# Optimization experiments

Hardware: AMD Instinct MI355X
Metric: run time of the kernel (lower is better)

Reference implementation:

```python
import jax, jax.numpy as jnp
import numpy as np

B, A = 64, 128          # batch, number of annotations (source length)
H, E, V = 512, 512, 32000  # hidden_size, embedding_size, vocab_size


def setup_inputs() -> dict:
    key = jax.random.key(0)
    ks = jax.random.split(key, 12)
    def w(k, shape):
        return (jax.random.normal(k, shape, jnp.float32) * 0.02)
    return {
        "hidden_state": jax.random.normal(ks[0], (B, H), jnp.float32),
        "annotations": jax.random.normal(ks[1], (B, A, 2 * H), jnp.float32),
        # Wa: Linear(3H -> H), ReLU, Linear(H -> 1)
        "Wa1_w": w(ks[2], (3 * H, H)), "Wa1_b": jnp.zeros((H,), jnp.float32),
        "Wa2_w": w(ks[3], (H, 1)),     "Wa2_b": jnp.zeros((1,), jnp.float32),
        # Wf: Linear(H+E+2H -> H//2), ReLU, Linear(H//2 -> H)
        "Wf1_w": w(ks[4], (H + E + 2 * H, H // 2)), "Wf1_b": jnp.zeros((H // 2,), jnp.float32),
        "Wf2_w": w(ks[5], (H // 2, H)),             "Wf2_b": jnp.zeros((H,), jnp.float32),
        # Wg: Linear(E+H+2H -> E//2), ReLU, Linear(E//2 -> E)
        "Wg1_w": w(ks[6], (E + H + 2 * H, E // 2)), "Wg1_b": jnp.zeros((E // 2,), jnp.float32),
        "Wg2_w": w(ks[7], (E // 2, E)),             "Wg2_b": jnp.zeros((E,), jnp.float32),
        # fc: Linear(E -> V)
        "fc_w": w(ks[8], (E, V)), "fc_b": jnp.zeros((V,), jnp.float32),
        "decode_length": 64,
    }


def reference(hidden_state, annotations,
              Wa1_w, Wa1_b, Wa2_w, Wa2_b,
              Wf1_w, Wf1_b, Wf2_w, Wf2_b,
              Wg1_w, Wg1_b, Wg2_w, Wg2_b,
              fc_w, fc_b, decode_length):
    h_dim = hidden_state.shape[-1]
    # concat([s, ann]) @ Wa1 is linear: precompute annotation part once (same math).
    ann_proj = jnp.einsum('bad,dh->bah', annotations, Wa1_w[h_dim:]) + Wa1_b  # [B,A,H]
    Wa1_s = Wa1_w[:h_dim]            # [H,H] part applied to the decoder state
    y0 = jnp.zeros((hidden_state.shape[0], Wg2_w.shape[1]), hidden_state.dtype)

    def step(carry, _):
        s, y = carry
        # attention energies: MLP on concat([s, annotation])
        hid = jax.nn.relu(jnp.einsum('bh,hk->bk', s, Wa1_s)[:, None, :] + ann_proj)  # [B,A,H]
        e = jnp.einsum('bah,h->ba', hid, Wa2_w[:, 0]) + Wa2_b[0]                     # [B,A]
        attn = jax.nn.softmax(e, axis=1)
        c = jnp.einsum('ba,bad->bd', attn, annotations)                              # [B,2H]
        # f: new hidden state
        s_new = jax.nn.relu(jnp.concatenate([s, y, c], -1) @ Wf1_w + Wf1_b) @ Wf2_w + Wf2_b
        # g: prediction embedding
        y_new = jax.nn.relu(jnp.concatenate([y, s_new, c], -1) @ Wg1_w + Wg1_b) @ Wg2_w + Wg2_b
        return (s_new, y_new), y_new

    _, ys = jax.lax.scan(step, (hidden_state, y0), None, length=decode_length)
    outputs = jnp.transpose(ys, (1, 0, 2))  # [B,T,E]
    return outputs @ fc_w + fc_b            # [B,T,V]
```

## Files before the change

kernel.cpp:

```cpp
#include <hip/hip_runtime.h>

typedef unsigned short US;
typedef unsigned int   UI;
typedef __bf16 bf16x8 __attribute__((ext_vector_type(8)));
typedef float  f32x4  __attribute__((ext_vector_type(4)));

#define BB 64
#define AA 128
#define HH 512
#define TT 64
#define VV 32000

__device__ __forceinline__ US f2bf(float f) {
  UI u = __builtin_bit_cast(UI, f);
  UI r = (u + 0x7fffu + ((u >> 16) & 1u)) >> 16;
  return (US)r;
}
__device__ __forceinline__ float bflo(UI u){ return __builtin_bit_cast(float, u << 16); }
__device__ __forceinline__ float bfhi(UI u){ return __builtin_bit_cast(float, u & 0xffff0000u); }

__device__ __forceinline__ float dot8(uint4 w, const float* __restrict__ x){
  float a = 0.f;
  a += x[0]*bflo(w.x); a += x[1]*bfhi(w.x);
  a += x[2]*bflo(w.y); a += x[3]*bfhi(w.y);
  a += x[4]*bflo(w.z); a += x[5]*bfhi(w.z);
  a += x[6]*bflo(w.w); a += x[7]*bfhi(w.w);
  return a;
}

__global__ void copy_f(float* o, const float* i, int n){
  int x = blockIdx.x*blockDim.x + threadIdx.x; if (x < n) o[x] = i[x];
}
__global__ void cast4_k(US* o, const float* in, int n4){
  int x = blockIdx.x*blockDim.x + threadIdx.x;
  if (x < n4){
    float4 v = ((const float4*)in)[x];
    ushort4 r; r.x=f2bf(v.x); r.y=f2bf(v.y); r.z=f2bf(v.z); r.w=f2bf(v.w);
    ((ushort4*)o)[x] = r;
  }
}
__global__ void tcast_k(US* __restrict__ out, const float* __restrict__ in,
                        int R, int C, int in_stride){
  __shared__ float tile[32][33];
  int r0 = blockIdx.x*32, c0 = blockIdx.y*32;
  int tx = threadIdx.x, ty = threadIdx.y;
  #pragma unroll
  for (int k=0;k<4;k++)
    tile[tx][ty+8*k] = in[(long)(c0+ty+8*k)*in_stride + r0 + tx];
  __syncthreads();
  #pragma unroll
  for (int k=0;k<4;k++)
    out[(long)(r0+ty+8*k)*C + c0 + tx] = f2bf(tile[ty+8*k][tx]);
}
__global__ void w2g_k(US* __restrict__ W2gT, const float* __restrict__ Wf2,
                      const float* __restrict__ Wg1){
  int j2 = blockIdx.x, j = threadIdx.x;
  float a = 0.f;
  for (int n=0;n<HH;n++) a += Wf2[j*HH + n] * Wg1[(512+n)*256 + j2];
  W2gT[j2*256 + j] = f2bf(a);
}
__global__ void bg1p_k(float* out, const float* Wg1_b, const float* Wf2_b,
                       const float* Wg1){
  int j2 = threadIdx.x;
  float a = Wg1_b[j2];
  for (int n=0;n<HH;n++) a += Wf2_b[n]*Wg1[(512+n)*256 + j2];
  out[j2] = a;
}

template<int OUT_BF16>
__global__ __launch_bounds__(256) void gemm_bt(
    const US* __restrict__ A, const US* __restrict__ Bt, void* __restrict__ Cv,
    const float* __restrict__ bias, int M, int N, int K,
    long Az, long Bz, long Cz)
{
  const long zb = blockIdx.z;
  A  += zb*Az;  Bt += zb*Bz;
  __shared__ __align__(16) US lA[128*64];
  __shared__ __align__(16) US lB[128*64];
  const int tid = threadIdx.x, lane = tid & 63, w = tid >> 6;
  const int wr = w >> 1, wc = w & 1;
  const int tm = blockIdx.x, tn = blockIdx.y;
  f32x4 acc[4][4] = {};
  for (int kt = 0; kt < K; kt += 64) {
    __syncthreads();
    #pragma unroll
    for (int i=0;i<4;i++){
      int ci = tid + 256*i; int r = ci>>3, o = (ci&7)*8;
      *(uint4*)&lA[r*64+o] = *(const uint4*)&A [(long)(tm*128+r)*K + kt + o];
      *(uint4*)&lB[r*64+o] = *(const uint4*)&Bt[(long)(tn*128+r)*K + kt + o];
    }
    __syncthreads();
    #pragma unroll
    for (int ks=0; ks<2; ++ks){
      bf16x8 af[4], bfr[4];
      #pragma unroll
      for(int m=0;m<4;m++){
        uint4 t = *(const uint4*)&lA[(wr*64+m*16+(lane&15))*64 + ks*32 + (lane>>4)*8];
        af[m] = __builtin_bit_cast(bf16x8, t);
      }
      #pragma unroll
      for(int n=0;n<4;n++){
        uint4 t = *(const uint4*)&lB[(wc*64+n*16+(lane&15))*64 + ks*32 + (lane>>4)*8];
        bfr[n] = __builtin_bit_cast(bf16x8, t);
      }
      #pragma unroll
      for(int m=0;m<4;m++)
        #pragma unroll
        for(int n=0;n<4;n++)
          acc[m][n] = __builtin_amdgcn_mfma_f32_16x16x32_bf16(af[m], bfr[n], acc[m][n], 0,0,0);
    }
  }
  #pragma unroll
  for(int m=0;m<4;m++){
    #pragma unroll
    for(int n=0;n<4;n++){
      const int col = tn*128 + wc*64 + n*16 + (lane&15);
      const float bv = bias ? bias[col] : 0.f;
      #pragma unroll
      for(int r=0;r<4;r++){
        const int row = tm*128 + wr*64 + m*16 + (lane>>4)*4 + r;
        const float v = acc[m][n][r] + bv;
        if (OUT_BF16) ((US*)Cv)  [zb*Cz + (long)row*N + col] = f2bf(v);
        else          ((float*)Cv)[zb*Cz + (long)row*N + col] = v;
      }
    }
  }
}

__device__ __forceinline__ void bbar(int* cnt, int target){
  __syncthreads();
  if (threadIdx.x == 0){
    __threadfence();
    __hip_atomic_fetch_add(cnt, 1, __ATOMIC_RELEASE, __HIP_MEMORY_SCOPE_AGENT);
    while (__hip_atomic_load(cnt, __ATOMIC_ACQUIRE, __HIP_MEMORY_SCOPE_AGENT) < target)
      __builtin_amdgcn_s_sleep(2);
  }
  __syncthreads();
}

__global__ __launch_bounds__(512) void scan_k(
  float* __restrict__ S, float* __restrict__ Y, float* __restrict__ TMP,
  float* __restrict__ E, float* __restrict__ U, float* __restrict__ V,
  int* __restrict__ cnt,
  const US* __restrict__ Wa1sT, const US* __restrict__ Wg2T,
  const US* __restrict__ annproj, const US* __restrict__ annFt, const US* __restrict__ annGt,
  const US* __restrict__ Wf1syT, const US* __restrict__ Wf2T,
  const US* __restrict__ Wg1yT, const US* __restrict__ W2gT,
  const float* __restrict__ bg1p, const float* __restrict__ wa2g,
  const float* __restrict__ Wf1_b, const float* __restrict__ Wf2_b,
  const float* __restrict__ Wg2_b,
  US* __restrict__ ys)
{
  const int b = blockIdx.x & 63, q = blockIdx.x >> 6;
  const int tid = threadIdx.x;
  __shared__ float s_l[512], y_l[512], tmp_l[512], v_l[256], u_l[256];
  __shared__ float p_l[128], aF_l[64], aG_l[64], wa2[512], red_l[4];
  wa2[tid] = wa2g[tid];
  float* Sb = S + b*512;  float* Yb = Y + b*512;  float* Tb = TMP + b*512;
  float* Eb = E + b*128;  float* Ub = U + b*256;  float* Vb = V + b*256;
  int* cb = cnt + b*32;
  int bt = 0;

  for (int t = 0; t <= TT; ++t) {
    if (t > 0 && tid < 256) v_l[tid] = Vb[tid];
    s_l[tid] = Sb[tid];
    __syncthreads();
    {
      const int n_loc = tid >> 2, kq = tid & 3;
      const int n = q*128 + n_loc;
      if (t > 0) {
        const US* wrow = Wg2T + n*256 + kq*64;
        const float* x = &v_l[kq*64];
        float p = 0.f;
        #pragma unroll
        for (int i=0;i<8;i++) p += dot8(*(const uint4*)&wrow[i*8], &x[i*8]);
        p += __shfl_xor(p, 1); p += __shfl_xor(p, 2);
        if (kq == 0) {
          float yv = p + Wg2_b[n];
          Yb[n] = yv;
          ys[((long)b*TT + (t-1))*512 + n] = f2bf(yv);
        }
      }
      if (t == TT) break;
      {
        const US* wrow = Wa1sT + n*512 + kq*128;
        const float* x = &s_l[kq*128];
        float p = 0.f;
        #pragma unroll
        for (int i=0;i<16;i++) p += dot8(*(const uint4*)&wrow[i*8], &x[i*8]);
        p += __shfl_xor(p, 1); p += __shfl_xor(p, 2);
        if (kq == 0) Tb[n] = p;
      }
    }
    bt += 4; bbar(cb, bt);

    tmp_l[tid] = Tb[tid];
    __syncthreads();
    {
      const int a_loc = tid >> 4, hq = tid & 15;
      const int a = q*32 + a_loc;
      const US* prow = annproj + ((long)b*AA + a)*512 + hq*32;
      float p = 0.f;
      #pragma unroll
      for (int i=0;i<4;i++){
        uint4 wv = *(const uint4*)&prow[i*8];
        const int h = hq*32 + i*8;
        float tv;
        tv = tmp_l[h+0]+bflo(wv.x); p += fmaxf(tv,0.f)*wa2[h+0];
        tv = tmp_l[h+1]+bfhi(wv.x); p += fmaxf(tv,0.f)*wa2[h+1];
        tv = tmp_l[h+2]+bflo(wv.y); p += fmaxf(tv,0.f)*wa2[h+2];
        tv = tmp_l[h+3]+bfhi(wv.y); p += fmaxf(tv,0.f)*wa2[h+3];
        tv = tmp_l[h+4]+bflo(wv.z); p += fmaxf(tv,0.f)*wa2[h+4];
        tv = tmp_l[h+5]+bfhi(wv.z); p += fmaxf(tv,0.f)*wa2[h+5];
        tv = tmp_l[h+6]+bflo(wv.w); p += fmaxf(tv,0.f)*wa2[h+6];
        tv = tmp_l[h+7]+bfhi(wv.w); p += fmaxf(tv,0.f)*wa2[h+7];
      }
      p += __shfl_xor(p,1); p += __shfl_xor(p,2); p += __shfl_xor(p,4); p += __shfl_xor(p,8);
      if (hq == 0) Eb[a] = p;
    }
    bt += 4; bbar(cb, bt);

    float ev = -1e30f;
    if (tid < 128){ ev = Eb[tid]; p_l[tid] = ev; }
    y_l[tid] = Yb[tid];
    __syncthreads();
    float mloc = ev;
    #pragma unroll
    for (int o=32;o;o>>=1) mloc = fmaxf(mloc, __shfl_xor(mloc,o));
    if (tid==0)  red_l[0]=mloc;
    if (tid==64) red_l[1]=mloc;
    __syncthreads();
    const float mx = fmaxf(red_l[0], red_l[1]);
    float dloc = 0.f;
    if (tid < 128){ float pe = expf(ev - mx); p_l[tid] = pe; dloc = pe; }
    #pragma unroll
    for (int o=32;o;o>>=1) dloc += __shfl_xor(dloc,o);
    if (tid==0)  red_l[2]=dloc;
    if (tid==64) red_l[3]=dloc;
    __syncthreads();
    const float dinv = 1.f/(red_l[2]+red_l[3]);
    {
      const int j_loc = tid>>3, aq = tid&7;
      const int j = q*64 + j_loc;
      const US* fr = annFt + ((long)b*256 + j)*AA + aq*16;
      const US* gr = annGt + ((long)b*256 + j)*AA + aq*16;
      float pF=0.f, pG=0.f;
      #pragma unroll
      for (int i=0;i<2;i++){
        pF += dot8(*(const uint4*)&fr[i*8], &p_l[aq*16 + i*8]);
        pG += dot8(*(const uint4*)&gr[i*8], &p_l[aq*16 + i*8]);
      }
      pF += __shfl_xor(pF,1); pF += __shfl_xor(pF,2); pF += __shfl_xor(pF,4);
      pG += __shfl_xor(pG,1); pG += __shfl_xor(pG,2); pG += __shfl_xor(pG,4);
      if (aq==0){ aF_l[j_loc]=pF; aG_l[j_loc]=pG; }
    }
    __syncthreads();
    {
      const int j_loc = tid>>3, kq = tid&7;
      const int j = q*64 + j_loc;
      const US* wrow = Wf1syT + (long)j*1024 + kq*128;
      float p = 0.f;
      #pragma unroll
      for (int i=0;i<16;i++){
        const int k = kq*128 + i*8;
        const float* x = (k < 512) ? &s_l[k] : &y_l[k-512];
        p += dot8(*(const uint4*)&wrow[i*8], x);
      }
      p += __shfl_xor(p,1); p += __shfl_xor(p,2); p += __shfl_xor(p,4);
      if (kq==0) Ub[j] = fmaxf(p + aF_l[j_loc]*dinv + Wf1_b[j], 0.f);
    }
    bt += 4; bbar(cb, bt);

    if (tid < 256) u_l[tid] = Ub[tid];
    __syncthreads();
    {
      const int n_loc = tid>>2, kq = tid&3;
      const int n = q*128 + n_loc;
      const US* wrow = Wf2T + n*256 + kq*64;
      const float* x = &u_l[kq*64];
      float p = 0.f;
      #pragma unroll
      for (int i=0;i<8;i++) p += dot8(*(const uint4*)&wrow[i*8], &x[i*8]);
      p += __shfl_xor(p,1); p += __shfl_xor(p,2);
      if (kq==0) Sb[n] = p + Wf2_b[n];
    }
    {
      const int j2_loc = tid>>3, kq = tid&7;
      const int j2 = q*64 + j2_loc;
      const US* wy = Wg1yT + (long)j2*512 + kq*64;
      const US* wu = W2gT + j2*256 + kq*32;
      float p = 0.f;
      #pragma unroll
      for (int i=0;i<8;i++) p += dot8(*(const uint4*)&wy[i*8], &y_l[kq*64 + i*8]);
      #pragma unroll
      for (int i=0;i<4;i++) p += dot8(*(const uint4*)&wu[i*8], &u_l[kq*32 + i*8]);
      p += __shfl_xor(p,1); p += __shfl_xor(p,2); p += __shfl_xor(p,4);
      if (kq==0) Vb[j2] = fmaxf(p + aG_l[j2_loc]*dinv + bg1p[j2], 0.f);
    }
    bt += 4; bbar(cb, bt);
  }
}

extern "C" void kernel_launch(void* const* d_in, const int* in_sizes, int n_in,
                              void* d_out, int out_size, void* d_ws, size_t ws_size,
                              hipStream_t stream)
{
  (void)in_sizes; (void)n_in; (void)out_size; (void)ws_size;
  const float* hidden = (const float*)d_in[0];
  const float* ann    = (const float*)d_in[1];
  const float* Wa1_w  = (const float*)d_in[2];
  const float* Wa1_b  = (const float*)d_in[3];
  const float* Wa2_w  = (const float*)d_in[4];
  const float* Wf1_w  = (const float*)d_in[6];
  const float* Wf1_b  = (const float*)d_in[7];
  const float* Wf2_w  = (const float*)d_in[8];
  const float* Wf2_b  = (const float*)d_in[9];
  const float* Wg1_w  = (const float*)d_in[10];
  const float* Wg1_b  = (const float*)d_in[11];
  const float* Wg2_w  = (const float*)d_in[12];
  const float* Wg2_b  = (const float*)d_in[13];
  const float* fc_w   = (const float*)d_in[14];
  const float* fc_b   = (const float*)d_in[15];

  char* ws = (char*)d_ws;
  size_t off = 0;
  auto alloc = [&](size_t bytes)->char*{ char* p = ws + off; off += (bytes + 255) & ~255ULL; return p; };
  int*   cnt   = (int*)  alloc(64*32*4);
  float* Y     = (float*)alloc(64*512*4);
  float* S     = (float*)alloc(64*512*4);
  float* TMP   = (float*)alloc(64*512*4);
  float* E     = (float*)alloc(64*128*4);
  float* U     = (float*)alloc(64*256*4);
  float* V     = (float*)alloc(64*256*4);
  float* BG1P  = (float*)alloc(256*4);
  US* Wa1sT  = (US*)alloc(512*512*2);
  US* WannT  = (US*)alloc(512*1024*2);
  US* Wf1cT  = (US*)alloc(256*1024*2);
  US* Wg1cT  = (US*)alloc(256*1024*2);
  US* Wf1syT = (US*)alloc(256*1024*2);
  US* Wf2T   = (US*)alloc(512*256*2);
  US* Wg1yT  = (US*)alloc(256*512*2);
  US* Wg2T   = (US*)alloc(512*256*2);
  US* W2gT   = (US*)alloc(256*256*2);
  US* annbf  = (US*)alloc((size_t)64*128*1024*2);
  US* annproj= (US*)alloc((size_t)64*128*512*2);
  US* annFt  = (US*)alloc((size_t)64*256*128*2);
  US* annGt  = (US*)alloc((size_t)64*256*128*2);
  US* ysbf   = (US*)alloc((size_t)64*64*512*2);
  US* fcwT   = (US*)alloc((size_t)32000*512*2);

  hipMemsetAsync(d_ws, 0, 64*32*4 + 64*512*4, stream);
  copy_f<<<64, 512, 0, stream>>>(S, hidden, 64*512);
  cast4_k<<<8192, 256, 0, stream>>>(annbf, ann, 64*128*1024/4);

  dim3 tb(32,8);
  tcast_k<<<dim3(16,16),  tb, 0, stream>>>(Wa1sT,  Wa1_w,            512, 512,  512);
  tcast_k<<<dim3(16,32),  tb, 0, stream>>>(WannT,  Wa1_w + 512*512,  512, 1024, 512);
  tcast_k<<<dim3(8,32),   tb, 0, stream>>>(Wf1cT,  Wf1_w + 1024*256, 256, 1024, 256);
  tcast_k<<<dim3(8,32),   tb, 0, stream>>>(Wg1cT,  Wg1_w + 1024*256, 256, 1024, 256);
  tcast_k<<<dim3(8,32),   tb, 0, stream>>>(Wf1syT, Wf1_w,            256, 1024, 256);
  tcast_k<<<dim3(16,8),   tb, 0, stream>>>(Wf2T,   Wf2_w,            512, 256,  512);
  tcast_k<<<dim3(8,16),   tb, 0, stream>>>(Wg1yT,  Wg1_w,            256, 512,  256);
  tcast_k<<<dim3(16,8),   tb, 0, stream>>>(Wg2T,   Wg2_w,            512, 256,  512);
  tcast_k<<<dim3(1000,16),tb, 0, stream>>>(fcwT,   fc_w,           32000, 512, 32000);
  w2g_k<<<256, 256, 0, stream>>>(W2gT, Wf2_w, Wg1_w);
  bg1p_k<<<1, 256, 0, stream>>>(BG1P, Wg1_b, Wf2_b, Wg1_w);

  gemm_bt<1><<<dim3(64,4,1), 256, 0, stream>>>(annbf, WannT, annproj, Wa1_b,
                                               8192, 512, 1024, 0, 0, 0);
  gemm_bt<1><<<dim3(2,1,64), 256, 0, stream>>>(Wf1cT, annbf, annFt, nullptr,
                                               256, 128, 1024, 0, 128*1024, 256*128);
  gemm_bt<1><<<dim3(2,1,64), 256, 0, stream>>>(Wg1cT, annbf, annGt, nullptr,
                                               256, 128, 1024, 0, 128*1024, 256*128);

  scan_k<<<256, 512, 0, stream>>>(S, Y, TMP, E, U, V, cnt,
                                  Wa1sT, Wg2T, annproj, annFt, annGt,
                                  Wf1syT, Wf2T, Wg1yT, W2gT,
                                  BG1P, Wa2_w, Wf1_b, Wf2_b, Wg2_b, ysbf);

  gemm_bt<0><<<dim3(32,250,1), 256, 0, stream>>>(ysbf, fcwT, d_out, fc_b,
                                                 4096, 32000, 512, 0, 0, 0);
}
```

Before: 10.05 ms.

## Run recurrent scan with one 1024-thread block per batch, dropping grid barriers

The scan kernel previously split each batch row across 4 blocks that synchronized through global atomic counters and exchanged state through global scratch buffers. Now a single 1024-thread block per batch keeps all state (s, y, tmp, u, v, attention) in shared memory and uses only __syncthreads. This removes the cross-block barrier latency and the global round trips on every step. The cost is that only 64 blocks run, and each thread now does more of the dot-product work serially, so per-step compute and weight bandwidth are spread across fewer CUs.

```diff
diff --git a/kernel.cpp b/kernel.cpp
--- a/kernel.cpp
+++ b/kernel.cpp
@@ -28,9 +28,6 @@
   return a;
 }
 
-__global__ void copy_f(float* o, const float* i, int n){
-  int x = blockIdx.x*blockDim.x + threadIdx.x; if (x < n) o[x] = i[x];
-}
 __global__ void cast4_k(US* o, const float* in, int n4){
   int x = blockIdx.x*blockDim.x + threadIdx.x;
   if (x < n4){
@@ -127,21 +124,8 @@
   }
 }
 
-__device__ __forceinline__ void bbar(int* cnt, int target){
-  __syncthreads();
-  if (threadIdx.x == 0){
-    __threadfence();
-    __hip_atomic_fetch_add(cnt, 1, __ATOMIC_RELEASE, __HIP_MEMORY_SCOPE_AGENT);
-    while (__hip_atomic_load(cnt, __ATOMIC_ACQUIRE, __HIP_MEMORY_SCOPE_AGENT) < target)
-      __builtin_amdgcn_s_sleep(2);
-  }
-  __syncthreads();
-}
-
-__global__ __launch_bounds__(512) void scan_k(
-  float* __restrict__ S, float* __restrict__ Y, float* __restrict__ TMP,
-  float* __restrict__ E, float* __restrict__ U, float* __restrict__ V,
-  int* __restrict__ cnt,
+__global__ __launch_bounds__(1024) void scan_k(
+  const float* __restrict__ hidden,
   const US* __restrict__ Wa1sT, const US* __restrict__ Wg2T,
   const US* __restrict__ annproj, const US* __restrict__ annFt, const US* __restrict__ annGt,
   const US* __restrict__ Wf1syT, const US* __restrict__ Wf2T,
@@ -151,60 +135,62 @@
   const float* __restrict__ Wg2_b,
   US* __restrict__ ys)
 {
-  const int b = blockIdx.x & 63, q = blockIdx.x >> 6;
+  const int b = blockIdx.x;
   const int tid = threadIdx.x;
   __shared__ float s_l[512], y_l[512], tmp_l[512], v_l[256], u_l[256];
-  __shared__ float p_l[128], aF_l[64], aG_l[64], wa2[512], red_l[4];
-  wa2[tid] = wa2g[tid];
-  float* Sb = S + b*512;  float* Yb = Y + b*512;  float* Tb = TMP + b*512;
-  float* Eb = E + b*128;  float* Ub = U + b*256;  float* Vb = V + b*256;
-  int* cb = cnt + b*32;
-  int bt = 0;
+  __shared__ float p_l[128], aF_l[256], aG_l[256];
+  __shared__ float wa2[512], gb2_l[512], fb1_l[256], fb2_l[512], bgp_l[256];
+  __shared__ float red_l[1];
+
+  if (tid < 512){
+    s_l[tid]  = hidden[b*512 + tid];
+    y_l[tid]  = 0.f;
+    wa2[tid]  = wa2g[tid];
+    gb2_l[tid]= Wg2_b[tid];
+    fb2_l[tid]= Wf2_b[tid];
+  } else {
+    int r = tid - 512;
+    if (r < 256){ fb1_l[r] = Wf1_b[r]; bgp_l[r] = bg1p[r]; }
+  }
+  __syncthreads();
 
   for (int t = 0; t <= TT; ++t) {
-    if (t > 0 && tid < 256) v_l[tid] = Vb[tid];
-    s_l[tid] = Sb[tid];
-    __syncthreads();
-    {
-      const int n_loc = tid >> 2, kq = tid & 3;
-      const int n = q*128 + n_loc;
+    {
+      const int n = tid >> 1, kq = tid & 1;
       if (t > 0) {
-        const US* wrow = Wg2T + n*256 + kq*64;
-        const float* x = &v_l[kq*64];
-        float p = 0.f;
-        #pragma unroll
-        for (int i=0;i<8;i++) p += dot8(*(const uint4*)&wrow[i*8], &x[i*8]);
-        p += __shfl_xor(p, 1); p += __shfl_xor(p, 2);
-        if (kq == 0) {
-          float yv = p + Wg2_b[n];
-          Yb[n] = yv;
-          ys[((long)b*TT + (t-1))*512 + n] = f2bf(yv);
-        }
-      }
-      if (t == TT) break;
-      {
-        const US* wrow = Wa1sT + n*512 + kq*128;
-        const float* x = &s_l[kq*128];
+        const US* wrow = Wg2T + n*256 + kq*128;
+        const float* x = &v_l[kq*128];
         float p = 0.f;
         #pragma unroll
         for (int i=0;i<16;i++) p += dot8(*(const uint4*)&wrow[i*8], &x[i*8]);
-        p += __shfl_xor(p, 1); p += __shfl_xor(p, 2);
-        if (kq == 0) Tb[n] = p;
-      }
-    }
-    bt += 4; bbar(cb, bt);
-
-    tmp_l[tid] = Tb[tid];
-    __syncthreads();
-    {
-      const int a_loc = tid >> 4, hq = tid & 15;
-      const int a = q*32 + a_loc;
-      const US* prow = annproj + ((long)b*AA + a)*512 + hq*32;
-      float p = 0.f;
-      #pragma unroll
-      for (int i=0;i<4;i++){
-        uint4 wv = *(const uint4*)&prow[i*8];
-        const int h = hq*32 + i*8;
+        p += __shfl_xor(p, 1);
+        if (kq == 0) {
+          float yv = p + gb2_l[n];
+          y_l[n] = yv;
+          ys[((long)b*TT + (t-1))*512 + n] = f2bf(yv);
+        }
+      }
+      if (t == TT) break;
+      {
+        const US* wrow = Wa1sT + n*512 + kq*256;
+        const float* x = &s_l[kq*256];
+        float p = 0.f;
+        #pragma unroll
+        for (int i=0;i<32;i++) p += dot8(*(const uint4*)&wrow[i*8], &x[i*8]);
+        p += __shfl_xor(p, 1);
+        if (kq == 0) tmp_l[n] = p;
+      }
+    }
+    __syncthreads();
+
+    {
+      const int a = tid >> 3, c = tid & 7;
+      const US* prow = annproj + ((long)b*AA + a)*512;
+      float p = 0.f;
+      #pragma unroll
+      for (int k=0;k<8;k++){
+        const int h = c*8 + k*64;
+        uint4 wv = *(const uint4*)&prow[h];
         float tv;
         tv = tmp_l[h+0]+bflo(wv.x); p += fmaxf(tv,0.f)*wa2[h+0];
         tv = tmp_l[h+1]+bfhi(wv.x); p += fmaxf(tv,0.f)*wa2[h+1];
@@ -215,89 +201,72 @@
         tv = tmp_l[h+6]+bflo(wv.w); p += fmaxf(tv,0.f)*wa2[h+6];
         tv = tmp_l[h+7]+bfhi(wv.w); p += fmaxf(tv,0.f)*wa2[h+7];
       }
-      p += __shfl_xor(p,1); p += __shfl_xor(p,2); p += __shfl_xor(p,4); p += __shfl_xor(p,8);
-      if (hq == 0) Eb[a] = p;
-    }
-    bt += 4; bbar(cb, bt);
-
-    float ev = -1e30f;
-    if (tid < 128){ ev = Eb[tid]; p_l[tid] = ev; }
-    y_l[tid] = Yb[tid];
-    __syncthreads();
-    float mloc = ev;
-    #pragma unroll
-    for (int o=32;o;o>>=1) mloc = fmaxf(mloc, __shfl_xor(mloc,o));
-    if (tid==0)  red_l[0]=mloc;
-    if (tid==64) red_l[1]=mloc;
-    __syncthreads();
-    const float mx = fmaxf(red_l[0], red_l[1]);
-    float dloc = 0.f;
-    if (tid < 128){ float pe = expf(ev - mx); p_l[tid] = pe; dloc = pe; }
-    #pragma unroll
-    for (int o=32;o;o>>=1) dloc += __shfl_xor(dloc,o);
-    if (tid==0)  red_l[2]=dloc;
-    if (tid==64) red_l[3]=dloc;
-    __syncthreads();
-    const float dinv = 1.f/(red_l[2]+red_l[3]);
-    {
-      const int j_loc = tid>>3, aq = tid&7;
-      const int j = q*64 + j_loc;
-      const US* fr = annFt + ((long)b*256 + j)*AA + aq*16;
-      const US* gr = annGt + ((long)b*256 + j)*AA + aq*16;
-      float pF=0.f, pG=0.f;
-      #pragma unroll
-      for (int i=0;i<2;i++){
-        pF += dot8(*(const uint4*)&fr[i*8], &p_l[aq*16 + i*8]);
-        pG += dot8(*(const uint4*)&gr[i*8], &p_l[aq*16 + i*8]);
-      }
-      pF += __shfl_xor(pF,1); pF += __shfl_xor(pF,2); pF += __shfl_xor(pF,4);
-      pG += __shfl_xor(pG,1); pG += __shfl_xor(pG,2); pG += __shfl_xor(pG,4);
-      if (aq==0){ aF_l[j_loc]=pF; aG_l[j_loc]=pG; }
-    }
-    __syncthreads();
-    {
-      const int j_loc = tid>>3, kq = tid&7;
-      const int j = q*64 + j_loc;
-      const US* wrow = Wf1syT + (long)j*1024 + kq*128;
-      float p = 0.f;
-      #pragma unroll
-      for (int i=0;i<16;i++){
-        const int k = kq*128 + i*8;
-        const float* x = (k < 512) ? &s_l[k] : &y_l[k-512];
-        p += dot8(*(const uint4*)&wrow[i*8], x);
-      }
       p += __shfl_xor(p,1); p += __shfl_xor(p,2); p += __shfl_xor(p,4);
-      if (kq==0) Ub[j] = fmaxf(p + aF_l[j_loc]*dinv + Wf1_b[j], 0.f);
-    }
-    bt += 4; bbar(cb, bt);
-
-    if (tid < 256) u_l[tid] = Ub[tid];
-    __syncthreads();
-    {
-      const int n_loc = tid>>2, kq = tid&3;
-      const int n = q*128 + n_loc;
-      const US* wrow = Wf2T + n*256 + kq*64;
-      const float* x = &u_l[kq*64];
-      float p = 0.f;
-      #pragma unroll
-      for (int i=0;i<8;i++) p += dot8(*(const uint4*)&wrow[i*8], &x[i*8]);
+      if (c == 0) p_l[a] = p;
+    }
+    __syncthreads();
+
+    if (tid < 64){
+      float e0 = p_l[tid], e1 = p_l[tid+64];
+      float m = fmaxf(e0,e1);
+      #pragma unroll
+      for (int o=32;o;o>>=1) m = fmaxf(m, __shfl_xor(m,o));
+      float p0 = expf(e0-m), p1 = expf(e1-m);
+      p_l[tid] = p0; p_l[tid+64] = p1;
+      float d = p0+p1;
+      #pragma unroll
+      for (int o=32;o;o>>=1) d += __shfl_xor(d,o);
+      if (tid==0) red_l[0] = 1.f/d;
+    }
+    __syncthreads();
+    const float dinv = red_l[0];
+
+    {
+      const int j = (tid & 511) >> 1, aq = tid & 1;
+      const US* base = ((tid < 512)? annFt : annGt) + ((long)b*256 + j)*AA + aq*64;
+      float p = 0.f;
+      #pragma unroll
+      for (int i=0;i<8;i++) p += dot8(*(const uint4*)&base[i*8], &p_l[aq*64 + i*8]);
+      p += __shfl_xor(p,1);
+      if (aq == 0){ if (tid < 512) aF_l[j] = p; else aG_l[j] = p; }
+    }
+    __syncthreads();
+
+    {
+      const int j = tid >> 2, c = tid & 3;
+      const US* wrow = Wf1syT + (long)j*1024 + c*256;
+      const float* x = (c < 2)? &s_l[c*256] : &y_l[(c-2)*256];
+      float p = 0.f;
+      #pragma unroll
+      for (int i=0;i<32;i++) p += dot8(*(const uint4*)&wrow[i*8], &x[i*8]);
       p += __shfl_xor(p,1); p += __shfl_xor(p,2);
-      if (kq==0) Sb[n] = p + Wf2_b[n];
-    }
-    {
-      const int j2_loc = tid>>3, kq = tid&7;
-      const int j2 = q*64 + j2_loc;
-      const US* wy = Wg1yT + (long)j2*512 + kq*64;
-      const US* wu = W2gT + j2*256 + kq*32;
-      float p = 0.f;
-      #pragma unroll
-      for (int i=0;i<8;i++) p += dot8(*(const uint4*)&wy[i*8], &y_l[kq*64 + i*8]);
-      #pragma unroll
-      for (int i=0;i<4;i++) p += dot8(*(const uint4*)&wu[i*8], &u_l[kq*32 + i*8]);
-      p += __shfl_xor(p,1); p += __shfl_xor(p,2); p += __shfl_xor(p,4);
-      if (kq==0) Vb[j2] = fmaxf(p + aG_l[j2_loc]*dinv + bg1p[j2], 0.f);
-    }
-    bt += 4; bbar(cb, bt);
+      if (c == 0) u_l[j] = fmaxf(p + aF_l[j]*dinv + fb1_l[j], 0.f);
+    }
+    __syncthreads();
+
+    {
+      const int n = tid >> 1, kq = tid & 1;
+      const US* wrow = Wf2T + n*256 + kq*128;
+      const float* x = &u_l[kq*128];
+      float p = 0.f;
+      #pragma unroll
+      for (int i=0;i<16;i++) p += dot8(*(const uint4*)&wrow[i*8], &x[i*8]);
+      p += __shfl_xor(p,1);
+      if (kq == 0) s_l[n] = p + fb2_l[n];
+    }
+    {
+      const int j2 = tid >> 2, c = tid & 3;
+      const US* wy = Wg1yT + (long)j2*512 + c*128;
+      const US* wu = W2gT  + j2*256 + c*64;
+      float p = 0.f;
+      #pragma unroll
+      for (int i=0;i<16;i++) p += dot8(*(const uint4*)&wy[i*8], &y_l[c*128 + i*8]);
+      #pragma unroll
+      for (int i=0;i<8;i++)  p += dot8(*(const uint4*)&wu[i*8], &u_l[c*64  + i*8]);
+      p += __shfl_xor(p,1); p += __shfl_xor(p,2);
+      if (c == 0) v_l[j2] = fmaxf(p + aG_l[j2]*dinv + bgp_l[j2], 0.f);
+    }
+    __syncthreads();
   }
 }
 
@@ -325,13 +294,6 @@
   char* ws = (char*)d_ws;
   size_t off = 0;
   auto alloc = [&](size_t bytes)->char*{ char* p = ws + off; off += (bytes + 255) & ~255ULL; return p; };
-  int*   cnt   = (int*)  alloc(64*32*4);
-  float* Y     = (float*)alloc(64*512*4);
-  float* S     = (float*)alloc(64*512*4);
-  float* TMP   = (float*)alloc(64*512*4);
-  float* E     = (float*)alloc(64*128*4);
-  float* U     = (float*)alloc(64*256*4);
-  float* V     = (float*)alloc(64*256*4);
   float* BG1P  = (float*)alloc(256*4);
   US* Wa1sT  = (US*)alloc(512*512*2);
   US* WannT  = (US*)alloc(512*1024*2);
@@ -349,8 +311,6 @@
   US* ysbf   = (US*)alloc((size_t)64*64*512*2);
   US* fcwT   = (US*)alloc((size_t)32000*512*2);
 
-  hipMemsetAsync(d_ws, 0, 64*32*4 + 64*512*4, stream);
-  copy_f<<<64, 512, 0, stream>>>(S, hidden, 64*512);
   cast4_k<<<8192, 256, 0, stream>>>(annbf, ann, 64*128*1024/4);
 
   dim3 tb(32,8);
@@ -373,7 +333,7 @@
   gemm_bt<1><<<dim3(2,1,64), 256, 0, stream>>>(Wg1cT, annbf, annGt, nullptr,
                                                256, 128, 1024, 0, 128*1024, 256*128);
 
-  scan_k<<<256, 512, 0, stream>>>(S, Y, TMP, E, U, V, cnt,
+  scan_k<<<64, 1024, 0, stream>>>(hidden,
                                   Wa1sT, Wg2T, annproj, annFt, annGt,
                                   Wf1syT, Wf2T, Wg1yT, W2gT,
                                   BG1P, Wa2_w, Wf1_b, Wf2_b, Wg2_b, ysbf);
```

New measurement: 20.48 ms. 2.04x slower.
